# Kernel tuning notes

Measured on AMD Instinct MI355X. Metric: run time of the kernel, lower is better.

## Reference

```python
import jax, jax.numpy as jnp
import numpy as np

DIM = 512
DEPTH = 4
HEADS = 8
MLP = 4096
HEAD_DIM = DIM // HEADS
SCALE = HEAD_DIM ** -0.5
EPS = 1e-5


def setup_inputs() -> dict:
    key = jax.random.key(0)
    ks = jax.random.split(key, 14)
    B, C, H, W, D = 1, DIM, 16, 16, 16
    x = jax.random.normal(ks[0], (B, C, H, W, D), dtype=jnp.float32)
    s = 0.02
    inp = {
        'x': x,
        # GroupNorm(1, C) affine params per layer
        'g1': jnp.ones((DEPTH, C), jnp.float32),
        'b1': jnp.zeros((DEPTH, C), jnp.float32),
        'g2': jnp.ones((DEPTH, C), jnp.float32),
        'b2': jnp.zeros((DEPTH, C), jnp.float32),
        # 1x1 conv weights act as channel matmuls
        'wq': jax.random.normal(ks[1], (DEPTH, C, C), jnp.float32) * s,
        'wk': jax.random.normal(ks[2], (DEPTH, C, C), jnp.float32) * s,
        'wv': jax.random.normal(ks[3], (DEPTH, C, C), jnp.float32) * s,
        'wp': jax.random.normal(ks[4], (DEPTH, C, C), jnp.float32) * s,
        'bp': jnp.zeros((DEPTH, C), jnp.float32),
        'w1': jax.random.normal(ks[5], (DEPTH, MLP, C), jnp.float32) * s,
        'bb1': jnp.zeros((DEPTH, MLP), jnp.float32),
        'w2': jax.random.normal(ks[6], (DEPTH, C, MLP), jnp.float32) * s,
        'bb2': jnp.zeros((DEPTH, C), jnp.float32),
    }
    return inp


def _groupnorm1(x, g, b):
    # GroupNorm(num_groups=1): normalize over (C,H,W,D) per sample, per-channel affine
    mu = jnp.mean(x, axis=(1, 2, 3, 4), keepdims=True)
    var = jnp.mean(jnp.square(x - mu), axis=(1, 2, 3, 4), keepdims=True)
    xn = (x - mu) * jax.lax.rsqrt(var + EPS)
    return xn * g[None, :, None, None, None] + b[None, :, None, None, None]


def _attention(x, wq, wk, wv, wp, bp):
    B, C, H, W, D = x.shape
    N = H * W * D
    xf = x.reshape(B, C, N)
    # 1x1 conv == channel matmul; then the module's non-standard view:
    # C split as (head_dim, num_heads)
    q = jnp.einsum('oc,bcn->bon', wq, xf).reshape(B, HEAD_DIM, HEADS, N)
    k = jnp.einsum('oc,bcn->bon', wk, xf).reshape(B, HEAD_DIM, HEADS, N)
    v = jnp.einsum('oc,bcn->bon', wv, xf).reshape(B, HEAD_DIM, HEADS, N)
    attn = jnp.einsum('bchn,bchm->bhnm', q, k) * SCALE  # [B,H,N,N]
    attn = jax.nn.softmax(attn, axis=-1)
    o = jnp.einsum('bhnm,bchm->bchn', attn, v).reshape(B, C, N)
    o = jnp.einsum('oc,bcn->bon', wp, o) + bp[None, :, None]
    return o.reshape(B, C, H, W, D)


def _feedforward(x, w1, bb1, w2, bb2):
    B, C, H, W, D = x.shape
    N = H * W * D
    xf = x.reshape(B, C, N)
    h = jax.nn.relu(jnp.einsum('mc,bcn->bmn', w1, xf) + bb1[None, :, None])
    o = jnp.einsum('cm,bmn->bcn', w2, h) + bb2[None, :, None]
    return o.reshape(B, C, H, W, D)


def reference(x, g1, b1, g2, b2, wq, wk, wv, wp, bp, w1, bb1, w2, bb2):
    for l in range(DEPTH):
        x = x + _attention(_groupnorm1(x, g1[l], b1[l]), wq[l], wk[l], wv[l], wp[l], bp[l])
        x = x + _feedforward(_groupnorm1(x, g2[l], b2[l]), w1[l], bb1[l], w2[l], bb2[l])
    return x
```

## Files before the change

### kernel.cpp

```cpp
#include <hip/hip_runtime.h>

#define CDIM   512
#define NTOK   4096
#define TOT    (CDIM*NTOK)
#define MLPD   4096
#define EPS    1e-5f
#define QSCALE 0.1803368801111204f

typedef _Float16 f16;
typedef _Float16 f16x8 __attribute__((ext_vector_type(8)));
typedef float    f32x4 __attribute__((ext_vector_type(4)));

typedef __attribute__((address_space(3))) void lds_void;
typedef const __attribute__((address_space(1))) void glb_void;

__device__ __forceinline__ void gload16(const void* g, void* l) {
  __builtin_amdgcn_global_load_lds((glb_void*)g, (lds_void*)l, 16, 0, 0);
}

__device__ __forceinline__ f32x4 zero4() { f32x4 z; z[0]=0.f; z[1]=0.f; z[2]=0.f; z[3]=0.f; return z; }

__global__ __launch_bounds__(256) void cvt_qkv(const float* __restrict__ wq,
                                               const float* __restrict__ wk,
                                               const float* __restrict__ wv,
                                               f16* __restrict__ dst) {
  int i = blockIdx.x * 256 + threadIdx.x;
  int k0 = (i & 63) * 8;
  int rowglob = i >> 6;
  int l = rowglob / 1536;
  int n = rowglob - l * 1536;
  int sect = n >> 9, nn = n & 511;
  int h = nn >> 6, hd = nn & 63;
  int c = hd * 8 + h;
  const float* base = (sect == 0) ? wq : (sect == 1) ? wk : wv;
  const float* src = base + (size_t)l * 262144 + c * 512 + k0;
  float scl = (sect == 0) ? QSCALE : 1.f;
  float4 a = *(const float4*)src;
  float4 b = *(const float4*)(src + 4);
  f16x8 o;
  o[0]=(f16)(a.x*scl); o[1]=(f16)(a.y*scl); o[2]=(f16)(a.z*scl); o[3]=(f16)(a.w*scl);
  o[4]=(f16)(b.x*scl); o[5]=(f16)(b.y*scl); o[6]=(f16)(b.z*scl); o[7]=(f16)(b.w*scl);
  *(f16x8*)&dst[(size_t)l * 786432 + (size_t)n * 512 + k0] = o;
}

__global__ __launch_bounds__(256) void cvt_wp(const float* __restrict__ wp,
                                              f16* __restrict__ dst) {
  int i = blockIdx.x * 256 + threadIdx.x;
  int d0 = (i & 63) * 8;
  int rowglob = i >> 6;
  int l = rowglob >> 9, n = rowglob & 511;
  int h = d0 >> 6;
  const float* src = wp + (size_t)l * 262144 + (size_t)n * 512;
  f16x8 o;
#pragma unroll
  for (int u = 0; u < 8; ++u) {
    int hd = (d0 + u) & 63;
    o[u] = (f16)src[hd * 8 + h];
  }
  *(f16x8*)&dst[(size_t)l * 262144 + (size_t)n * 512 + d0] = o;
}

__global__ __launch_bounds__(256) void cvt_12(const float* __restrict__ w1,
                                              const float* __restrict__ w2,
                                              f16* __restrict__ d1,
                                              f16* __restrict__ d2) {
  int i = blockIdx.x * 256 + threadIdx.x;
  const float* src = blockIdx.y ? w2 : w1;
  f16* dst = blockIdx.y ? d2 : d1;
  size_t e = (size_t)i * 8;
  float4 a = *(const float4*)(src + e);
  float4 b = *(const float4*)(src + e + 4);
  f16x8 o;
  o[0]=(f16)a.x; o[1]=(f16)a.y; o[2]=(f16)a.z; o[3]=(f16)a.w;
  o[4]=(f16)b.x; o[5]=(f16)b.y; o[6]=(f16)b.z; o[7]=(f16)b.w;
  *(f16x8*)&dst[e] = o;
}

template <bool STATS>
__global__ __launch_bounds__(256) void transpose_k(const float* __restrict__ src,
                                                   float* __restrict__ dst,
                                                   int R, int C,
                                                   float* __restrict__ stats) {
  __shared__ float t[64][65];
  int c0 = blockIdx.x * 64, r0 = blockIdx.y * 64;
  float s = 0.f, q = 0.f;
  for (int id = threadIdx.x; id < 1024; id += 256) {
    int row = id >> 4, cc = id & 15;
    float4 v = *(const float4*)&src[(size_t)(r0 + row) * C + c0 + cc * 4];
    *(float4*)&t[row][cc * 4] = v;
    if (STATS) {
      s += (v.x + v.y) + (v.z + v.w);
      q += (v.x*v.x + v.y*v.y) + (v.z*v.z + v.w*v.w);
    }
  }
  __syncthreads();
  for (int id = threadIdx.x; id < 1024; id += 256) {
    int row = id >> 4, cc = id & 15;
    float4 o;
    o.x = t[cc*4+0][row]; o.y = t[cc*4+1][row];
    o.z = t[cc*4+2][row]; o.w = t[cc*4+3][row];
    *(float4*)&dst[(size_t)(c0 + row) * R + r0 + cc * 4] = o;
  }
  if (STATS) {
#pragma unroll
    for (int off = 32; off > 0; off >>= 1) {
      s += __shfl_down(s, off);
      q += __shfl_down(q, off);
    }
    if ((threadIdx.x & 63) == 0) {
      atomicAdd(&stats[0], s);
      atomicAdd(&stats[1], q);
    }
  }
}

__global__ __launch_bounds__(256) void gn_apply2(const float* __restrict__ x,
                                                 const float* __restrict__ stats,
                                                 const float* __restrict__ g,
                                                 const float* __restrict__ b,
                                                 f16* __restrict__ out) {
  int i = blockIdx.x * 256 + threadIdx.x;
  float mu = stats[0] * (1.f / TOT);
  float var = stats[1] * (1.f / TOT) - mu * mu;
  float rs = rsqrtf(var + EPS);
  int c0 = (i & 63) * 8;
  const float4* x4 = (const float4*)x;
  float4 a = x4[i * 2], c = x4[i * 2 + 1];
  float4 G0 = *(const float4*)(g + c0);
  float4 G1 = *(const float4*)(g + c0 + 4);
  float4 B0 = *(const float4*)(b + c0);
  float4 B1 = *(const float4*)(b + c0 + 4);
  f16x8 o;
  o[0]=(f16)((a.x-mu)*rs*G0.x+B0.x); o[1]=(f16)((a.y-mu)*rs*G0.y+B0.y);
  o[2]=(f16)((a.z-mu)*rs*G0.z+B0.z); o[3]=(f16)((a.w-mu)*rs*G0.w+B0.w);
  o[4]=(f16)((c.x-mu)*rs*G1.x+B1.x); o[5]=(f16)((c.y-mu)*rs*G1.y+B1.y);
  o[6]=(f16)((c.z-mu)*rs*G1.z+B1.z); o[7]=(f16)((c.w-mu)*rs*G1.w+B1.w);
  *(f16x8*)&out[(size_t)i * 8] = o;
}

template <int BM, int BN, int MODE>
__global__ __launch_bounds__(256) void hgemm2(const f16* __restrict__ A,
                                              const f16* __restrict__ Bw,
                                              const float* __restrict__ bias,
                                              f16* __restrict__ Cf16,
                                              float* __restrict__ Cf32,
                                              float* __restrict__ stats,
                                              int N, int K) {
  constexpr int MB = BM / 32, NB = BN / 32;
  __shared__ __align__(16) f16 SM[(BM + BN) * 64];
  f16* As = SM;
  f16* Bs = SM + BM * 64;

  const int tid = threadIdx.x;
  const int lane = tid & 63, wid = tid >> 6;
  const int wm = wid >> 1, wn = wid & 1;
  const int m0 = blockIdx.y * BM, n0 = blockIdx.x * BN;
  const int l15 = lane & 15, hi = lane >> 4;

  f32x4 acc[MB][NB];
#pragma unroll
  for (int mb = 0; mb < MB; ++mb)
#pragma unroll
    for (int nb = 0; nb < NB; ++nb) acc[mb][nb] = zero4();

  for (int k0 = 0; k0 < K; k0 += 64) {
#pragma unroll
    for (int j = 0; j < BM / 32; ++j) {
      int flat = j * 256 + tid;
      int row = flat >> 3, c = flat & 7;
      gload16(&A[(size_t)(m0 + row) * K + k0 + ((c ^ (row & 7)) * 8)],
              &As[(j * 256 + wid * 64) * 8]);
    }
#pragma unroll
    for (int j = 0; j < BN / 32; ++j) {
      int flat = j * 256 + tid;
      int row = flat >> 3, c = flat & 7;
      gload16(&Bw[(size_t)(n0 + row) * K + k0 + ((c ^ (row & 7)) * 8)],
              &Bs[(j * 256 + wid * 64) * 8]);
    }
    asm volatile("s_waitcnt vmcnt(0)" ::: "memory");
    __syncthreads();
#pragma unroll
    for (int ks = 0; ks < 2; ++ks) {
      f16x8 af[MB], bf[NB];
#pragma unroll
      for (int mb = 0; mb < MB; ++mb) {
        int row = wm * (BM / 2) + mb * 16 + l15;
        af[mb] = *(const f16x8*)&As[row * 64 + ((ks * 32 + hi * 8) ^ ((row & 7) * 8))];
      }
#pragma unroll
      for (int nb = 0; nb < NB; ++nb) {
        int row = wn * (BN / 2) + nb * 16 + l15;
        bf[nb] = *(const f16x8*)&Bs[row * 64 + ((ks * 32 + hi * 8) ^ ((row & 7) * 8))];
      }
#pragma unroll
      for (int mb = 0; mb < MB; ++mb)
#pragma unroll
        for (int nb = 0; nb < NB; ++nb)
          acc[mb][nb] = __builtin_amdgcn_mfma_f32_16x16x32_f16(af[mb], bf[nb], acc[mb][nb], 0, 0, 0);
    }
    __syncthreads();
  }

  if constexpr (MODE <= 1) {
    f16* Co = SM;
#pragma unroll
    for (int mb = 0; mb < MB; ++mb)
#pragma unroll
      for (int nb = 0; nb < NB; ++nb) {
        int colb = wn * (BN / 2) + nb * 16 + l15;
        float bv = 0.f;
        if constexpr (MODE == 1) bv = bias[n0 + colb];
#pragma unroll
        for (int r = 0; r < 4; ++r) {
          int row = wm * (BM / 2) + mb * 16 + hi * 4 + r;
          float v = acc[mb][nb][r];
          if constexpr (MODE == 1) v = fmaxf(v + bv, 0.f);
          Co[row * BN + (colb ^ ((row & 7) * 8))] = (f16)v;
        }
      }
    __syncthreads();
#pragma unroll
    for (int j = 0; j < BM * BN / 2048; ++j) {
      int flat = j * 256 + tid;
      int row = flat / (BN / 8), c = flat % (BN / 8);
      f16x8 v = *(const f16x8*)&Co[row * BN + ((c * 8) ^ ((row & 7) * 8))];
      *(f16x8*)&Cf16[(size_t)(m0 + row) * N + n0 + c * 8] = v;
    }
  } else {
    float* Co = (float*)SM;
#pragma unroll
    for (int mb = 0; mb < MB; ++mb)
#pragma unroll
      for (int nb = 0; nb < NB; ++nb) {
        int colb = wn * 32 + nb * 16 + l15;
#pragma unroll
        for (int r = 0; r < 4; ++r) {
          int row = wm * 32 + mb * 16 + hi * 4 + r;
          Co[row * 64 + (colb ^ ((row & 7) * 4))] = acc[mb][nb][r];
        }
      }
    __syncthreads();
    float s_acc = 0.f, q_acc = 0.f;
#pragma unroll
    for (int j = 0; j < 4; ++j) {
      int flat = j * 256 + tid;
      int row = flat >> 4, c = flat & 15;
      float4 v = *(const float4*)&Co[row * 64 + ((c * 4) ^ ((row & 7) * 4))];
      float4 b4 = *(const float4*)&bias[n0 + c * 4];
      float* gp = &Cf32[(size_t)(m0 + row) * N + n0 + c * 4];
      float4 old = *(const float4*)gp;
      float4 rr;
      rr.x = old.x + v.x + b4.x; rr.y = old.y + v.y + b4.y;
      rr.z = old.z + v.z + b4.z; rr.w = old.w + v.w + b4.w;
      *(float4*)gp = rr;
      s_acc += (rr.x + rr.y) + (rr.z + rr.w);
      q_acc += (rr.x*rr.x + rr.y*rr.y) + (rr.z*rr.z + rr.w*rr.w);
    }
#pragma unroll
    for (int off = 32; off > 0; off >>= 1) {
      s_acc += __shfl_down(s_acc, off);
      q_acc += __shfl_down(q_acc, off);
    }
    if (lane == 0) {
      atomicAdd(&stats[0], s_acc);
      atomicAdd(&stats[1], q_acc);
    }
  }
}

__global__ __launch_bounds__(256) void perm_v2(const f16* __restrict__ qkv,
                                               f16* __restrict__ vc) {
  __shared__ f16 t[64][72];
  int t0 = blockIdx.x * 64, c0 = blockIdx.y * 64;
  for (int id = threadIdx.x; id < 512; id += 256) {
    int row = id >> 3, cc = id & 7;
    *(f16x8*)&t[row][cc * 8] =
        *(const f16x8*)&qkv[(size_t)(t0 + row) * 1536 + 1024 + c0 + cc * 8];
  }
  __syncthreads();
  for (int id = threadIdx.x; id < 512; id += 256) {
    int row = id >> 3, cc = id & 7;
    f16x8 o;
#pragma unroll
    for (int u = 0; u < 8; ++u) o[u] = t[cc * 8 + u][row];
    *(f16x8*)&vc[(size_t)(c0 + row) * NTOK + t0 + cc * 8] = o;
  }
}

__global__ __launch_bounds__(256) void attn2(const f16* __restrict__ qkv,
                                             const f16* __restrict__ vc,
                                             f16* __restrict__ o) {
  __shared__ __align__(16) f16 Ks[2][128 * 64];
  __shared__ __align__(16) f16 Vs[2][64 * 128];
  __shared__ __align__(16) f16 Ps[64 * 128];

  const int tid = threadIdx.x;
  const int lane = tid & 63, w = tid >> 6;
  const int l15 = lane & 15, hi = lane >> 4;
  const int h = blockIdx.y, q0 = blockIdx.x * 64;

  const f16* qrow = qkv + (size_t)(q0 + w * 16 + l15) * 1536 + h * 64;
  f16x8 qf0 = *(const f16x8*)(qrow + hi * 8);
  f16x8 qf1 = *(const f16x8*)(qrow + 32 + hi * 8);

  float l_run[4] = {0.f, 0.f, 0.f, 0.f};
  f32x4 oacc[4];
#pragma unroll
  for (int nbh = 0; nbh < 4; ++nbh) oacc[nbh] = zero4();

  auto stageK = [&](int buf, int kb) {
#pragma unroll
    for (int j = 0; j < 4; ++j) {
      int flat = j * 256 + tid;
      int rho = flat >> 3, c = flat & 7;
      int key = kb * 128 + ((rho & 15) * 8 + (rho >> 4));
      gload16(qkv + (size_t)key * 1536 + 512 + h * 64 + ((c ^ (rho & 7)) * 8),
              &Ks[buf][(j * 256 + w * 64) * 8]);
    }
  };
  auto stageV = [&](int buf, int kb) {
#pragma unroll
    for (int j = 0; j < 4; ++j) {
      int flat = j * 256 + tid;
      int hd = flat >> 4, c = flat & 15;
      gload16(vc + (size_t)(h * 64 + hd) * NTOK + kb * 128 + ((c ^ (hd & 7)) * 8),
              &Vs[buf][(j * 256 + w * 64) * 8]);
    }
  };

  stageK(0, 0); stageV(0, 0);
  asm volatile("s_waitcnt vmcnt(0)" ::: "memory");
  __syncthreads();

  for (int kb = 0; kb < 32; ++kb) {
    int cur = kb & 1;
    if (kb < 31) { stageK(cur ^ 1, kb + 1); stageV(cur ^ 1, kb + 1); }

    const f16* Kb = &Ks[cur][0];
    f32x4 sacc[8];
#pragma unroll
    for (int nb = 0; nb < 8; ++nb) sacc[nb] = zero4();
#pragma unroll
    for (int nb = 0; nb < 8; ++nb) {
      int row = nb * 16 + l15;
      int sw = (row & 7) * 8;
      f16x8 k0f = *(const f16x8*)&Kb[row * 64 + ((hi * 8) ^ sw)];
      f16x8 k1f = *(const f16x8*)&Kb[row * 64 + ((32 + hi * 8) ^ sw)];
      sacc[nb] = __builtin_amdgcn_mfma_f32_16x16x32_f16(qf0, k0f, sacc[nb], 0, 0, 0);
      sacc[nb] = __builtin_amdgcn_mfma_f32_16x16x32_f16(qf1, k1f, sacc[nb], 0, 0, 0);
    }

#pragma unroll
    for (int r = 0; r < 4; ++r) {
      int prow = w * 16 + hi * 4 + r;
      f16x8 pv;
      float ps = 0.f;
#pragma unroll
      for (int nb = 0; nb < 8; ++nb) {
        float p = exp2f(sacc[nb][r]);
        ps += p;
        pv[nb] = (f16)p;
      }
      *(f16x8*)&Ps[prow * 128 + ((l15 ^ (prow & 7)) * 8)] = pv;
#pragma unroll
      for (int off = 1; off < 16; off <<= 1) ps += __shfl_xor(ps, off);
      l_run[r] += ps;
    }

    const f16* Vb = &Vs[cur][0];
    {
      int prow = w * 16 + l15;
      int psw = (prow & 7) * 8;
#pragma unroll
      for (int ks2 = 0; ks2 < 4; ++ks2) {
        f16x8 pf = *(const f16x8*)&Ps[prow * 128 + ((ks2 * 32 + hi * 8) ^ psw)];
#pragma unroll
        for (int nbh = 0; nbh < 4; ++nbh) {
          int vrow = nbh * 16 + l15;
          f16x8 vf = *(const f16x8*)&Vb[vrow * 128 + ((ks2 * 32 + hi * 8) ^ ((vrow & 7) * 8))];
          oacc[nbh] = __builtin_amdgcn_mfma_f32_16x16x32_f16(pf, vf, oacc[nbh], 0, 0, 0);
        }
      }
    }
    asm volatile("s_waitcnt vmcnt(0)" ::: "memory");
    __syncthreads();
  }

  float inv[4];
#pragma unroll
  for (int r = 0; r < 4; ++r) inv[r] = 1.f / l_run[r];
  f16* Ot = Ps;
#pragma unroll
  for (int r = 0; r < 4; ++r) {
    int row = w * 16 + hi * 4 + r;
    int sw = (row & 7) * 8;
#pragma unroll
    for (int nbh = 0; nbh < 4; ++nbh) {
      int col = nbh * 16 + l15;
      Ot[row * 64 + (col ^ sw)] = (f16)(oacc[nbh][r] * inv[r]);
    }
  }
  __syncthreads();
#pragma unroll
  for (int j = 0; j < 2; ++j) {
    int flat = j * 256 + tid;
    int row = flat >> 3, c = flat & 7;
    f16x8 v = *(const f16x8*)&Ot[row * 64 + ((c ^ (row & 7)) * 8)];
    *(f16x8*)&o[(size_t)(q0 + row) * 512 + h * 64 + c * 8] = v;
  }
}

extern "C" void kernel_launch(void* const* d_in, const int* in_sizes, int n_in,
                              void* d_out, int out_size, void* d_ws, size_t ws_size,
                              hipStream_t stream) {
  const float* x   = (const float*)d_in[0];
  const float* g1  = (const float*)d_in[1];
  const float* b1  = (const float*)d_in[2];
  const float* g2  = (const float*)d_in[3];
  const float* b2  = (const float*)d_in[4];
  const float* wq  = (const float*)d_in[5];
  const float* wk  = (const float*)d_in[6];
  const float* wv  = (const float*)d_in[7];
  const float* wp  = (const float*)d_in[8];
  const float* bp  = (const float*)d_in[9];
  const float* w1  = (const float*)d_in[10];
  const float* bb1 = (const float*)d_in[11];
  const float* w2  = (const float*)d_in[12];
  const float* bb2 = (const float*)d_in[13];

  char* base = (char*)d_ws;
  size_t off = 0;
  f16* wqkvF = (f16*)(base + off); off += (size_t)4 * 786432 * 2;
  f16* wpF   = (f16*)(base + off); off += (size_t)4 * 262144 * 2;
  f16* w1F   = (f16*)(base + off); off += (size_t)4 * 2097152 * 2;
  f16* w2F   = (f16*)(base + off); off += (size_t)4 * 2097152 * 2;
  float* xcur = (float*)(base + off); off += (size_t)TOT * 4;
  f16* xnT   = (f16*)(base + off); off += (size_t)TOT * 2;
  float* stats_raw = (float*)(base + off); off += 256;
  char* U = base + off; off += 33554432;
  f16* qkvT = (f16*)U;
  f16* vc2  = (f16*)(U + 12582912);
  f16* oatt = (f16*)(U + 16777216);
  f16* hT   = (f16*)U;

  if (ws_size < off) return;

  hipMemsetAsync(stats_raw, 0, 18 * sizeof(float), stream);

  cvt_qkv<<<1536, 256, 0, stream>>>(wq, wk, wv, wqkvF);
  cvt_wp<<<512, 256, 0, stream>>>(wp, wpF);
  cvt_12<<<dim3(4096, 2), 256, 0, stream>>>(w1, w2, w1F, w2F);

  transpose_k<true><<<dim3(64, 8), 256, 0, stream>>>(x, xcur, 512, 4096, stats_raw);

  for (int l = 0; l < 4; ++l) {
    gn_apply2<<<1024, 256, 0, stream>>>(xcur, stats_raw + 2 * (2 * l),
                                        g1 + l * CDIM, b1 + l * CDIM, xnT);
    hgemm2<128, 128, 0><<<dim3(12, 32), 256, 0, stream>>>(
        xnT, wqkvF + (size_t)l * 786432, nullptr, qkvT, nullptr, nullptr, 1536, 512);
    perm_v2<<<dim3(64, 8), 256, 0, stream>>>(qkvT, vc2);
    attn2<<<dim3(64, 8), 256, 0, stream>>>(qkvT, vc2, oatt);
    hgemm2<64, 64, 2><<<dim3(8, 64), 256, 0, stream>>>(
        oatt, wpF + (size_t)l * 262144, bp + l * CDIM, nullptr, xcur,
        stats_raw + 2 * (2 * l + 1), 512, 512);

    gn_apply2<<<1024, 256, 0, stream>>>(xcur, stats_raw + 2 * (2 * l + 1),
                                        g2 + l * CDIM, b2 + l * CDIM, xnT);
    hgemm2<128, 128, 1><<<dim3(32, 32), 256, 0, stream>>>(
        xnT, w1F + (size_t)l * 2097152, bb1 + l * MLPD, hT, nullptr, nullptr, 4096, 512);
    hgemm2<64, 64, 2><<<dim3(8, 64), 256, 0, stream>>>(
        hT, w2F + (size_t)l * 2097152, bb2 + l * CDIM, nullptr, xcur,
        stats_raw + 2 * (2 * l + 2), 512, 4096);
  }

  transpose_k<false><<<dim3(8, 64), 256, 0, stream>>>(xcur, (float*)d_out, 4096, 512, nullptr);
}
```

Before: 1.403 ms.

## Shrink attention key tiles, add MFMA priority hints, widen residual GEMM tiles

The attention kernel now processes keys in blocks of 64 instead of 128, which halves its LDS use (likely raising occupancy) at the cost of twice as many loop iterations and barriers. It also raises wave priority around the MFMA sections with s_setprio. The residual-GEMM epilogue writes accumulators straight to global memory with per-element read-modify-write, skipping the LDS staging and barrier but giving up float4-coalesced accesses. The residual GEMMs switch to 64x128 tiles, so half as many blocks are launched.

```diff
diff --git a/kernel.cpp b/kernel.cpp
--- a/kernel.cpp
+++ b/kernel.cpp
@@ -8,6 +8,7 @@
 #define QSCALE 0.1803368801111204f
 
 typedef _Float16 f16;
+typedef _Float16 f16x4 __attribute__((ext_vector_type(4)));
 typedef _Float16 f16x8 __attribute__((ext_vector_type(8)));
 typedef float    f32x4 __attribute__((ext_vector_type(4)));
 
@@ -228,34 +229,24 @@
       *(f16x8*)&Cf16[(size_t)(m0 + row) * N + n0 + c * 8] = v;
     }
   } else {
-    float* Co = (float*)SM;
-#pragma unroll
-    for (int mb = 0; mb < MB; ++mb)
+    float s_acc = 0.f, q_acc = 0.f;
+    const int rbase = m0 + wm * (BM / 2) + hi * 4;
+#pragma unroll
+    for (int mb = 0; mb < MB; ++mb) {
 #pragma unroll
       for (int nb = 0; nb < NB; ++nb) {
-        int colb = wn * 32 + nb * 16 + l15;
+        int col = n0 + wn * (BN / 2) + nb * 16 + l15;
+        float bv = bias[col];
 #pragma unroll
         for (int r = 0; r < 4; ++r) {
-          int row = wm * 32 + mb * 16 + hi * 4 + r;
-          Co[row * 64 + (colb ^ ((row & 7) * 4))] = acc[mb][nb][r];
+          int row = rbase + mb * 16 + r;
+          float* gp = &Cf32[(size_t)row * N + col];
+          float rr = *gp + acc[mb][nb][r] + bv;
+          *gp = rr;
+          s_acc += rr;
+          q_acc += rr * rr;
         }
       }
-    __syncthreads();
-    float s_acc = 0.f, q_acc = 0.f;
-#pragma unroll
-    for (int j = 0; j < 4; ++j) {
-      int flat = j * 256 + tid;
-      int row = flat >> 4, c = flat & 15;
-      float4 v = *(const float4*)&Co[row * 64 + ((c * 4) ^ ((row & 7) * 4))];
-      float4 b4 = *(const float4*)&bias[n0 + c * 4];
-      float* gp = &Cf32[(size_t)(m0 + row) * N + n0 + c * 4];
-      float4 old = *(const float4*)gp;
-      float4 rr;
-      rr.x = old.x + v.x + b4.x; rr.y = old.y + v.y + b4.y;
-      rr.z = old.z + v.z + b4.z; rr.w = old.w + v.w + b4.w;
-      *(float4*)gp = rr;
-      s_acc += (rr.x + rr.y) + (rr.z + rr.w);
-      q_acc += (rr.x*rr.x + rr.y*rr.y) + (rr.z*rr.z + rr.w*rr.w);
     }
 #pragma unroll
     for (int off = 32; off > 0; off >>= 1) {
@@ -291,9 +282,9 @@
 __global__ __launch_bounds__(256) void attn2(const f16* __restrict__ qkv,
                                              const f16* __restrict__ vc,
                                              f16* __restrict__ o) {
-  __shared__ __align__(16) f16 Ks[2][128 * 64];
-  __shared__ __align__(16) f16 Vs[2][64 * 128];
-  __shared__ __align__(16) f16 Ps[64 * 128];
+  __shared__ __align__(16) f16 Ks[2][64 * 64];
+  __shared__ __align__(16) f16 Vs[2][64 * 64];
+  __shared__ __align__(16) f16 Ps[64 * 64];
 
   const int tid = threadIdx.x;
   const int lane = tid & 63, w = tid >> 6;
@@ -311,20 +302,20 @@
 
   auto stageK = [&](int buf, int kb) {
 #pragma unroll
-    for (int j = 0; j < 4; ++j) {
+    for (int j = 0; j < 2; ++j) {
       int flat = j * 256 + tid;
       int rho = flat >> 3, c = flat & 7;
-      int key = kb * 128 + ((rho & 15) * 8 + (rho >> 4));
+      int key = kb * 64 + ((rho & 15) * 4 + (rho >> 4));
       gload16(qkv + (size_t)key * 1536 + 512 + h * 64 + ((c ^ (rho & 7)) * 8),
               &Ks[buf][(j * 256 + w * 64) * 8]);
     }
   };
   auto stageV = [&](int buf, int kb) {
 #pragma unroll
-    for (int j = 0; j < 4; ++j) {
+    for (int j = 0; j < 2; ++j) {
       int flat = j * 256 + tid;
-      int hd = flat >> 4, c = flat & 15;
-      gload16(vc + (size_t)(h * 64 + hd) * NTOK + kb * 128 + ((c ^ (hd & 7)) * 8),
+      int hd = flat >> 3, c = flat & 7;
+      gload16(vc + (size_t)(h * 64 + hd) * NTOK + kb * 64 + ((c ^ (hd & 7)) * 8),
               &Vs[buf][(j * 256 + w * 64) * 8]);
     }
   };
@@ -333,16 +324,17 @@
   asm volatile("s_waitcnt vmcnt(0)" ::: "memory");
   __syncthreads();
 
-  for (int kb = 0; kb < 32; ++kb) {
+  for (int kb = 0; kb < 64; ++kb) {
     int cur = kb & 1;
-    if (kb < 31) { stageK(cur ^ 1, kb + 1); stageV(cur ^ 1, kb + 1); }
+    if (kb < 63) { stageK(cur ^ 1, kb + 1); stageV(cur ^ 1, kb + 1); }
 
     const f16* Kb = &Ks[cur][0];
-    f32x4 sacc[8];
-#pragma unroll
-    for (int nb = 0; nb < 8; ++nb) sacc[nb] = zero4();
-#pragma unroll
-    for (int nb = 0; nb < 8; ++nb) {
+    f32x4 sacc[4];
+#pragma unroll
+    for (int nb = 0; nb < 4; ++nb) sacc[nb] = zero4();
+    __builtin_amdgcn_s_setprio(1);
+#pragma unroll
+    for (int nb = 0; nb < 4; ++nb) {
       int row = nb * 16 + l15;
       int sw = (row & 7) * 8;
       f16x8 k0f = *(const f16x8*)&Kb[row * 64 + ((hi * 8) ^ sw)];
@@ -350,19 +342,20 @@
       sacc[nb] = __builtin_amdgcn_mfma_f32_16x16x32_f16(qf0, k0f, sacc[nb], 0, 0, 0);
       sacc[nb] = __builtin_amdgcn_mfma_f32_16x16x32_f16(qf1, k1f, sacc[nb], 0, 0, 0);
     }
+    __builtin_amdgcn_s_setprio(0);
 
 #pragma unroll
     for (int r = 0; r < 4; ++r) {
       int prow = w * 16 + hi * 4 + r;
-      f16x8 pv;
+      f16x4 pv;
       float ps = 0.f;
 #pragma unroll
-      for (int nb = 0; nb < 8; ++nb) {
+      for (int nb = 0; nb < 4; ++nb) {
         float p = exp2f(sacc[nb][r]);
         ps += p;
         pv[nb] = (f16)p;
       }
-      *(f16x8*)&Ps[prow * 128 + ((l15 ^ (prow & 7)) * 8)] = pv;
+      *(f16x4*)&Ps[prow * 64 + ((l15 * 4) ^ ((prow & 7) * 8))] = pv;
 #pragma unroll
       for (int off = 1; off < 16; off <<= 1) ps += __shfl_xor(ps, off);
       l_run[r] += ps;
@@ -372,16 +365,18 @@
     {
       int prow = w * 16 + l15;
       int psw = (prow & 7) * 8;
-#pragma unroll
-      for (int ks2 = 0; ks2 < 4; ++ks2) {
-        f16x8 pf = *(const f16x8*)&Ps[prow * 128 + ((ks2 * 32 + hi * 8) ^ psw)];
+      __builtin_amdgcn_s_setprio(1);
+#pragma unroll
+      for (int ks2 = 0; ks2 < 2; ++ks2) {
+        f16x8 pf = *(const f16x8*)&Ps[prow * 64 + ((ks2 * 32 + hi * 8) ^ psw)];
 #pragma unroll
         for (int nbh = 0; nbh < 4; ++nbh) {
           int vrow = nbh * 16 + l15;
-          f16x8 vf = *(const f16x8*)&Vb[vrow * 128 + ((ks2 * 32 + hi * 8) ^ ((vrow & 7) * 8))];
+          f16x8 vf = *(const f16x8*)&Vb[vrow * 64 + ((ks2 * 32 + hi * 8) ^ ((vrow & 7) * 8))];
           oacc[nbh] = __builtin_amdgcn_mfma_f32_16x16x32_f16(pf, vf, oacc[nbh], 0, 0, 0);
         }
       }
+      __builtin_amdgcn_s_setprio(0);
     }
     asm volatile("s_waitcnt vmcnt(0)" ::: "memory");
     __syncthreads();
@@ -461,7 +456,7 @@
         xnT, wqkvF + (size_t)l * 786432, nullptr, qkvT, nullptr, nullptr, 1536, 512);
     perm_v2<<<dim3(64, 8), 256, 0, stream>>>(qkvT, vc2);
     attn2<<<dim3(64, 8), 256, 0, stream>>>(qkvT, vc2, oatt);
-    hgemm2<64, 64, 2><<<dim3(8, 64), 256, 0, stream>>>(
+    hgemm2<64, 128, 2><<<dim3(4, 64), 256, 0, stream>>>(
         oatt, wpF + (size_t)l * 262144, bp + l * CDIM, nullptr, xcur,
         stats_raw + 2 * (2 * l + 1), 512, 512);
 
@@ -469,7 +464,7 @@
                                         g2 + l * CDIM, b2 + l * CDIM, xnT);
     hgemm2<128, 128, 1><<<dim3(32, 32), 256, 0, stream>>>(
         xnT, w1F + (size_t)l * 2097152, bb1 + l * MLPD, hT, nullptr, nullptr, 4096, 512);
-    hgemm2<64, 64, 2><<<dim3(8, 64), 256, 0, stream>>>(
+    hgemm2<64, 128, 2><<<dim3(4, 64), 256, 0, stream>>>(
         hT, w2F + (size_t)l * 2097152, bb2 + l * CDIM, nullptr, xcur,
         stats_raw + 2 * (2 * l + 2), 512, 4096);
   }
```

After: 1.294 ms. 1.08x faster.
